# Performance work log

Measured on AMD Instinct MI355X. Metric: run time of the kernel, lower is better.

Reference implementation:

```python
import jax, jax.numpy as jnp
import numpy as np

B, H, L, D = 4, 16, 1024, 64
DROP_P = 0.5


def setup_inputs() -> dict:
    key = jax.random.key(0)
    kq, kk, kv, kg, kd = jax.random.split(key, 5)
    q = jax.random.normal(kq, (B, H, L, D), dtype=jnp.float32)
    k = jax.random.normal(kk, (B, H, L, D), dtype=jnp.float32)
    v = jax.random.normal(kv, (B, H, L, D), dtype=jnp.float32)
    # standard Gumbel(0,1) noise consumed by gumbel_softmax
    gumbel_noise = jax.random.gumbel(kg, (B, H, L, L), dtype=jnp.float32)
    # inverted-dropout mask: keep w.p. (1-p), scale kept by 1/(1-p)
    keep = jax.random.bernoulli(kd, 1.0 - DROP_P, (B, H, L, L))
    drop_mask = keep.astype(jnp.float32) / (1.0 - DROP_P)
    return {"q": q, "k": k, "v": v, "gumbel_noise": gumbel_noise, "drop_mask": drop_mask}


def reference(q, k, v, gumbel_noise, drop_mask):
    q = jax.nn.elu(q)
    k = jax.nn.elu(k)
    v = jax.nn.elu(v)
    scale = q.shape[-1] ** -0.5  # qk / sqrt(d)
    qk = jnp.einsum("bhld,bhmd->bhlm", q, k) * scale
    # gumbel_softmax(hard=True), tau=1
    logits = qk + gumbel_noise
    y_soft = jax.nn.softmax(logits, axis=-1)
    y_hard = jax.nn.one_hot(jnp.argmax(y_soft, axis=-1), logits.shape[-1], dtype=y_soft.dtype)
    y = jax.lax.stop_gradient(y_hard - y_soft) + y_soft  # straight-through
    dropped = y * drop_mask  # dropout p=0.5
    out = jnp.einsum("bhlm,bhmd->bhld", dropped, v)
    return out
```

## Files before the change

### kernel.cpp

```cpp
#include <hip/hip_runtime.h>
#include <math.h>


#define BH    64
#define SEQ   1024
#define DIM   64
#define LT    128
#define MT    128
#define NTHR  256

typedef short bf16x8 __attribute__((ext_vector_type(8)));
typedef float f32x16 __attribute__((ext_vector_type(16)));

__device__ __forceinline__ float eluf(float x) { return x > 0.0f ? x : expm1f(x); }

__device__ __forceinline__ unsigned f2bf_bits(float x) {
    unsigned u = __float_as_uint(x);
    return (u + 0x7fffu + ((u >> 16) & 1u)) >> 16;
}

__device__ __forceinline__ void top2_update(float v, int m,
                                            float& b1, int& i1,
                                            float& b2, int& i2) {
    bool gt1 = (v > b1) || (v == b1 && m < i1);
    bool gt2 = (v > b2) || (v == b2 && m < i2);
    float nb2 = gt1 ? b1 : (gt2 ? v : b2);
    int   ni2 = gt1 ? i1 : (gt2 ? m : i2);
    b1 = gt1 ? v : b1;
    i1 = gt1 ? m : i1;
    b2 = nb2; i2 = ni2;
}

__device__ __forceinline__ void stage_tile(const float4* __restrict__ src4,
                                           short* __restrict__ hi,
                                           short* __restrict__ lo,
                                           int tid) {
    #pragma unroll
    for (int i = 0; i < 8; ++i) {
        int f = tid + NTHR * i;
        int row = f >> 4, qd = f & 15;
        float4 val = src4[row * 16 + qd];
        float e0 = eluf(val.x), e1 = eluf(val.y), e2 = eluf(val.z), e3 = eluf(val.w);
        unsigned h0 = f2bf_bits(e0), h1 = f2bf_bits(e1), h2 = f2bf_bits(e2), h3 = f2bf_bits(e3);
        unsigned l0b = f2bf_bits(e0 - __uint_as_float(h0 << 16));
        unsigned l1b = f2bf_bits(e1 - __uint_as_float(h1 << 16));
        unsigned l2b = f2bf_bits(e2 - __uint_as_float(h2 << 16));
        unsigned l3b = f2bf_bits(e3 - __uint_as_float(h3 << 16));
        short4 hv = make_short4((short)h0, (short)h1, (short)h2, (short)h3);
        short4 lv = make_short4((short)l0b, (short)l1b, (short)l2b, (short)l3b);
        int off = row * 64 + ((((qd >> 1) ^ (row & 7)) << 3)) + ((qd & 1) << 2);
        *(short4*)&hi[off] = hv;
        *(short4*)&lo[off] = lv;
    }
}

__global__ __launch_bounds__(NTHR, 2)
void fused_gumbel_attn(const float* __restrict__ q,
                       const float* __restrict__ k,
                       const float* __restrict__ v,
                       const float* __restrict__ gum,
                       const float* __restrict__ drop,
                       float* __restrict__ out) {
    __shared__ __align__(16) short qhi[LT * DIM];
    __shared__ __align__(16) short qlo[LT * DIM];
    __shared__ __align__(16) short khi[MT * DIM];
    __shared__ __align__(16) short klo[MT * DIM];
    __shared__ int   m1s[LT], m2s[LT], msf[LT];
    __shared__ float dropv[LT];

    const int tid  = threadIdx.x;
    const int w    = tid >> 6;
    const int lane = tid & 63;
    const int lrow = lane & 31;
    const int half = lane >> 5;
    const int bh   = blockIdx.x >> 3;
    const int l0   = (blockIdx.x & 7) * LT;
    const size_t rowbase = (size_t)(bh * SEQ + l0);

    stage_tile((const float4*)q + rowbase * 16, qhi, qlo, tid);

    float best1[16], best2[16];
    int   idx1[16], idx2[16];
    #pragma unroll
    for (int r = 0; r < 16; ++r) {
        best1[r] = -INFINITY; best2[r] = -INFINITY; idx1[r] = 0; idx2[r] = 0;
    }

    const float* gumrow = gum + (((size_t)(bh * SEQ + l0 + w * 32 + half * 4)) << 10) + lrow;

    const int aswz = lrow & 7;

    for (int mt = 0; mt < SEQ / MT; ++mt) {
        const int m0 = mt * MT;
        __syncthreads();
        stage_tile((const float4*)k + (size_t)(bh * SEQ + m0) * 16, khi, klo, tid);
        __syncthreads();

        float ga[16], gb[16];
        #pragma unroll
        for (int r = 0; r < 16; ++r) {
            int roff = ((r & 3) + 8 * (r >> 2)) << 10;
            ga[r] = gumrow[roff + m0];
            gb[r] = gumrow[roff + m0 + 32];
        }

        f32x16 acc[4];
        #pragma unroll
        for (int t = 0; t < 4; ++t) acc[t] = (f32x16)0.0f;

        #pragma unroll
        for (int ks = 0; ks < 4; ++ks) {
            const int o = ks * 2 + half;
            const int arow = w * 32 + lrow;
            bf16x8 a_hi = *(const bf16x8*)&qhi[arow * 64 + ((o ^ aswz) << 3)];
            bf16x8 a_lo = *(const bf16x8*)&qlo[arow * 64 + ((o ^ aswz) << 3)];
            #pragma unroll
            for (int t = 0; t < 4; ++t) {
                const int brow = t * 32 + lrow;
                bf16x8 b_hi = *(const bf16x8*)&khi[brow * 64 + ((o ^ aswz) << 3)];
                bf16x8 b_lo = *(const bf16x8*)&klo[brow * 64 + ((o ^ aswz) << 3)];
                acc[t] = __builtin_amdgcn_mfma_f32_32x32x16_bf16(a_hi, b_hi, acc[t], 0, 0, 0);
                acc[t] = __builtin_amdgcn_mfma_f32_32x32x16_bf16(a_hi, b_lo, acc[t], 0, 0, 0);
                acc[t] = __builtin_amdgcn_mfma_f32_32x32x16_bf16(a_lo, b_hi, acc[t], 0, 0, 0);
            }
        }

        #pragma unroll
        for (int r = 0; r < 16; ++r) {
            float lg = fmaf(acc[0][r], 0.125f, ga[r]);
            top2_update(lg, m0 + lrow, best1[r], idx1[r], best2[r], idx2[r]);
        }
        #pragma unroll
        for (int r = 0; r < 16; ++r) {
            int roff = ((r & 3) + 8 * (r >> 2)) << 10;
            ga[r] = gumrow[roff + m0 + 64];
        }
        #pragma unroll
        for (int r = 0; r < 16; ++r) {
            float lg = fmaf(acc[1][r], 0.125f, gb[r]);
            top2_update(lg, m0 + 32 + lrow, best1[r], idx1[r], best2[r], idx2[r]);
        }
        #pragma unroll
        for (int r = 0; r < 16; ++r) {
            int roff = ((r & 3) + 8 * (r >> 2)) << 10;
            gb[r] = gumrow[roff + m0 + 96];
        }
        #pragma unroll
        for (int r = 0; r < 16; ++r) {
            float lg = fmaf(acc[2][r], 0.125f, ga[r]);
            top2_update(lg, m0 + 64 + lrow, best1[r], idx1[r], best2[r], idx2[r]);
        }
        #pragma unroll
        for (int r = 0; r < 16; ++r) {
            float lg = fmaf(acc[3][r], 0.125f, gb[r]);
            top2_update(lg, m0 + 96 + lrow, best1[r], idx1[r], best2[r], idx2[r]);
        }
    }

    #pragma unroll
    for (int r = 0; r < 16; ++r) {
        #pragma unroll
        for (int s = 1; s < 32; s <<= 1) {
            float ob1 = __shfl_xor(best1[r], s);
            int   oi1 = __shfl_xor(idx1[r], s);
            float ob2 = __shfl_xor(best2[r], s);
            int   oi2 = __shfl_xor(idx2[r], s);
            top2_update(ob1, oi1, best1[r], idx1[r], best2[r], idx2[r]);
            top2_update(ob2, oi2, best1[r], idx1[r], best2[r], idx2[r]);
        }
    }
    if (lrow == 0) {
        #pragma unroll
        for (int r = 0; r < 16; ++r) {
            int local_row = w * 32 + (r & 3) + 8 * (r >> 2) + 4 * half;
            m1s[local_row] = idx1[r];
            m2s[local_row] = idx2[r];
        }
    }
    __syncthreads();

    {
        const int row  = tid >> 1;
        const int cand = tid & 1;
        const int m    = cand ? m2s[row] : m1s[row];
        const float4* q4r = (const float4*)q + (rowbase + row) * 16;
        const float4* k4r = (const float4*)k + (size_t)(bh * SEQ + m) * 16;
        double s = 0.0;
        #pragma unroll
        for (int i = 0; i < 16; ++i) {
            float4 a = q4r[i], b = k4r[i];
            s += (double)eluf(a.x) * (double)eluf(b.x);
            s += (double)eluf(a.y) * (double)eluf(b.y);
            s += (double)eluf(a.z) * (double)eluf(b.z);
            s += (double)eluf(a.w) * (double)eluf(b.w);
        }
        double L = s * 0.125 + (double)gum[((rowbase + row) << 10) + m];
        double Lo = __shfl_xor(L, 1);
        int    mo = __shfl_xor(m, 1);
        int mstar = (L > Lo || (L == Lo && m < mo)) ? m : mo;
        if (cand == 0) {
            msf[row]   = mstar;
            dropv[row] = drop[((rowbase + row) << 10) + mstar];
        }
    }
    __syncthreads();

    const float4* v4  = (const float4*)v + (size_t)(bh * SEQ) * 16;
    float4*       o4  = (float4*)out + rowbase * 16;
    #pragma unroll
    for (int i = 0; i < 8; ++i) {
        int f = tid + NTHR * i;
        int row = f >> 4, qd = f & 15;
        int m = msf[row];
        float dm = dropv[row];
        float4 vv = v4[m * 16 + qd];
        float4 ov;
        ov.x = dm * eluf(vv.x); ov.y = dm * eluf(vv.y);
        ov.z = dm * eluf(vv.z); ov.w = dm * eluf(vv.w);
        o4[row * 16 + qd] = ov;
    }
}

extern "C" void kernel_launch(void* const* d_in, const int* in_sizes, int n_in,
                              void* d_out, int out_size, void* d_ws, size_t ws_size,
                              hipStream_t stream) {
    const float* q    = (const float*)d_in[0];
    const float* k    = (const float*)d_in[1];
    const float* v    = (const float*)d_in[2];
    const float* gum  = (const float*)d_in[3];
    const float* drop = (const float*)d_in[4];
    float* out = (float*)d_out;

    fused_gumbel_attn<<<dim3(BH * (SEQ / LT)), dim3(NTHR), 0, stream>>>(
        q, k, v, gum, drop, out);
}
```

Baseline: 605.7 us.

## Split fused kernel into K-prep, register-pipelined score/top2, and fixup kernels

Replaces the single fused kernel with three launches. The first converts ELU(K) into hi/lo bf16 halves once, into workspace. The second gives each wave a 32-row Q tile held in registers and a quarter of the key range, and double-buffers K fragments and gumbel loads straight from global memory with no LDS or block barriers. The third merges the per-split top-2 candidates, rescores them in double precision, and writes the output. This is meant to remove the per-tile K restaging, the syncthreads stalls and the redundant ELU/split work. The cost is extra launches, a workspace round trip, and a tie-break simplified to strict greater-than.

```diff
diff --git a/kernel.cpp b/kernel.cpp
--- a/kernel.cpp
+++ b/kernel.cpp
@@ -2,12 +2,13 @@
 #include <math.h>
 
 
-#define BH    64
-#define SEQ   1024
-#define DIM   64
-#define LT    128
-#define MT    128
-#define NTHR  256
+#define BH      64
+#define SEQ     1024
+#define DIM     64
+#define NSPLIT  4
+#define MR      (SEQ / NSPLIT)
+#define NTILES  (MR / 32)
+#define NTHR    256
 
 typedef short bf16x8 __attribute__((ext_vector_type(8)));
 typedef float f32x16 __attribute__((ext_vector_type(16)));
@@ -19,11 +20,18 @@
     return (u + 0x7fffu + ((u >> 16) & 1u)) >> 16;
 }
 
+__device__ __forceinline__ void split_bf16(float x, short& h, short& l) {
+    unsigned hb = f2bf_bits(x);
+    float hf = __uint_as_float(hb << 16);
+    h = (short)hb;
+    l = (short)f2bf_bits(x - hf);
+}
+
 __device__ __forceinline__ void top2_update(float v, int m,
                                             float& b1, int& i1,
                                             float& b2, int& i2) {
-    bool gt1 = (v > b1) || (v == b1 && m < i1);
-    bool gt2 = (v > b2) || (v == b2 && m < i2);
+    bool gt1 = v > b1;
+    bool gt2 = v > b2;
     float nb2 = gt1 ? b1 : (gt2 ? v : b2);
     int   ni2 = gt1 ? i1 : (gt2 ? m : i2);
     b1 = gt1 ? v : b1;
@@ -31,193 +39,189 @@
     b2 = nb2; i2 = ni2;
 }
 
-__device__ __forceinline__ void stage_tile(const float4* __restrict__ src4,
-                                           short* __restrict__ hi,
-                                           short* __restrict__ lo,
-                                           int tid) {
-    #pragma unroll
-    for (int i = 0; i < 8; ++i) {
-        int f = tid + NTHR * i;
-        int row = f >> 4, qd = f & 15;
-        float4 val = src4[row * 16 + qd];
-        float e0 = eluf(val.x), e1 = eluf(val.y), e2 = eluf(val.z), e3 = eluf(val.w);
-        unsigned h0 = f2bf_bits(e0), h1 = f2bf_bits(e1), h2 = f2bf_bits(e2), h3 = f2bf_bits(e3);
-        unsigned l0b = f2bf_bits(e0 - __uint_as_float(h0 << 16));
-        unsigned l1b = f2bf_bits(e1 - __uint_as_float(h1 << 16));
-        unsigned l2b = f2bf_bits(e2 - __uint_as_float(h2 << 16));
-        unsigned l3b = f2bf_bits(e3 - __uint_as_float(h3 << 16));
-        short4 hv = make_short4((short)h0, (short)h1, (short)h2, (short)h3);
-        short4 lv = make_short4((short)l0b, (short)l1b, (short)l2b, (short)l3b);
-        int off = row * 64 + ((((qd >> 1) ^ (row & 7)) << 3)) + ((qd & 1) << 2);
-        *(short4*)&hi[off] = hv;
-        *(short4*)&lo[off] = lv;
-    }
-}
-
-__global__ __launch_bounds__(NTHR, 2)
-void fused_gumbel_attn(const float* __restrict__ q,
-                       const float* __restrict__ k,
-                       const float* __restrict__ v,
+__global__ __launch_bounds__(NTHR)
+void prep_k_kernel(const float4* __restrict__ k4,
+                   short4* __restrict__ khi, short4* __restrict__ klo) {
+    int f = blockIdx.x * NTHR + threadIdx.x;
+    float4 val = k4[f];
+    short4 hv, lv;
+    split_bf16(eluf(val.x), hv.x, lv.x);
+    split_bf16(eluf(val.y), hv.y, lv.y);
+    split_bf16(eluf(val.z), hv.z, lv.z);
+    split_bf16(eluf(val.w), hv.w, lv.w);
+    khi[f] = hv;
+    klo[f] = lv;
+}
+
+__global__ __launch_bounds__(NTHR, 3)
+void score_top2_kernel(const float* __restrict__ q,
+                       const short* __restrict__ khi,
+                       const short* __restrict__ klo,
                        const float* __restrict__ gum,
-                       const float* __restrict__ drop,
-                       float* __restrict__ out) {
-    __shared__ __align__(16) short qhi[LT * DIM];
-    __shared__ __align__(16) short qlo[LT * DIM];
-    __shared__ __align__(16) short khi[MT * DIM];
-    __shared__ __align__(16) short klo[MT * DIM];
-    __shared__ int   m1s[LT], m2s[LT], msf[LT];
-    __shared__ float dropv[LT];
-
-    const int tid  = threadIdx.x;
-    const int w    = tid >> 6;
-    const int lane = tid & 63;
+                       int4* __restrict__ top2out) {
+    const int w    = threadIdx.x >> 6;
+    const int lane = threadIdx.x & 63;
     const int lrow = lane & 31;
     const int half = lane >> 5;
-    const int bh   = blockIdx.x >> 3;
-    const int l0   = (blockIdx.x & 7) * LT;
-    const size_t rowbase = (size_t)(bh * SEQ + l0);
-
-    stage_tile((const float4*)q + rowbase * 16, qhi, qlo, tid);
-
-    float best1[16], best2[16];
-    int   idx1[16], idx2[16];
-    #pragma unroll
-    for (int r = 0; r < 16; ++r) {
-        best1[r] = -INFINITY; best2[r] = -INFINITY; idx1[r] = 0; idx2[r] = 0;
-    }
-
-    const float* gumrow = gum + (((size_t)(bh * SEQ + l0 + w * 32 + half * 4)) << 10) + lrow;
-
-    const int aswz = lrow & 7;
-
-    for (int mt = 0; mt < SEQ / MT; ++mt) {
-        const int m0 = mt * MT;
-        __syncthreads();
-        stage_tile((const float4*)k + (size_t)(bh * SEQ + m0) * 16, khi, klo, tid);
-        __syncthreads();
-
-        float ga[16], gb[16];
+
+    const int x     = blockIdx.x & 7;
+    const int j     = blockIdx.x >> 3;
+    const int bh    = x * 8 + (j & 7);
+    const int ltile = j >> 3;
+    const int l0    = ltile * 32;
+    const int ms    = w * MR;
+
+    const size_t row = (size_t)bh * SEQ + l0 + lrow;
+
+    bf16x8 qh[4], ql[4];
+    {
+        const float4* q4 = (const float4*)q + row * 16;
+        #pragma unroll
+        for (int ks = 0; ks < 4; ++ks) {
+            float4 a = q4[ks * 4 + half * 2];
+            float4 b = q4[ks * 4 + half * 2 + 1];
+            float e[8] = { eluf(a.x), eluf(a.y), eluf(a.z), eluf(a.w),
+                           eluf(b.x), eluf(b.y), eluf(b.z), eluf(b.w) };
+            #pragma unroll
+            for (int t = 0; t < 8; ++t) {
+                short h, l;
+                split_bf16(e[t], h, l);
+                qh[ks][t] = h;
+                ql[ks][t] = l;
+            }
+        }
+    }
+
+    const short* kh_base = khi + ((size_t)(bh * SEQ + ms + lrow) * 64 + half * 8);
+    const short* kl_base = klo + ((size_t)(bh * SEQ + ms + lrow) * 64 + half * 8);
+    const float* gp      = gum + (row << 10) + ms + half * 4;
+
+    float b1 = -INFINITY, b2 = -INFINITY;
+    int   i1 = 0, i2 = 0;
+
+    bf16x8 ah[2][4], al[2][4];
+    float  g[2][16];
+
+    #pragma unroll
+    for (int ks = 0; ks < 4; ++ks) {
+        ah[0][ks] = *(const bf16x8*)(kh_base + ks * 16);
+        al[0][ks] = *(const bf16x8*)(kl_base + ks * 16);
+    }
+    #pragma unroll
+    for (int qd = 0; qd < 4; ++qd) {
+        float4 t4 = *(const float4*)(gp + qd * 8);
+        g[0][qd * 4 + 0] = t4.x; g[0][qd * 4 + 1] = t4.y;
+        g[0][qd * 4 + 2] = t4.z; g[0][qd * 4 + 3] = t4.w;
+    }
+
+    #pragma unroll
+    for (int t = 0; t < NTILES; ++t) {
+        const int cur = t & 1, nxt = cur ^ 1;
+        if (t < NTILES - 1) {
+            #pragma unroll
+            for (int ks = 0; ks < 4; ++ks) {
+                ah[nxt][ks] = *(const bf16x8*)(kh_base + (t + 1) * 2048 + ks * 16);
+                al[nxt][ks] = *(const bf16x8*)(kl_base + (t + 1) * 2048 + ks * 16);
+            }
+            #pragma unroll
+            for (int qd = 0; qd < 4; ++qd) {
+                float4 t4 = *(const float4*)(gp + (t + 1) * 32 + qd * 8);
+                g[nxt][qd * 4 + 0] = t4.x; g[nxt][qd * 4 + 1] = t4.y;
+                g[nxt][qd * 4 + 2] = t4.z; g[nxt][qd * 4 + 3] = t4.w;
+            }
+        }
+
+        f32x16 acc = (f32x16)0.0f;
+        #pragma unroll
+        for (int ks = 0; ks < 4; ++ks) {
+            acc = __builtin_amdgcn_mfma_f32_32x32x16_bf16(ah[cur][ks], qh[ks], acc, 0, 0, 0);
+            acc = __builtin_amdgcn_mfma_f32_32x32x16_bf16(ah[cur][ks], ql[ks], acc, 0, 0, 0);
+            acc = __builtin_amdgcn_mfma_f32_32x32x16_bf16(al[cur][ks], qh[ks], acc, 0, 0, 0);
+        }
+
+        const int mb = ms + t * 32 + half * 4;
         #pragma unroll
         for (int r = 0; r < 16; ++r) {
-            int roff = ((r & 3) + 8 * (r >> 2)) << 10;
-            ga[r] = gumrow[roff + m0];
-            gb[r] = gumrow[roff + m0 + 32];
-        }
-
-        f32x16 acc[4];
-        #pragma unroll
-        for (int t = 0; t < 4; ++t) acc[t] = (f32x16)0.0f;
-
-        #pragma unroll
-        for (int ks = 0; ks < 4; ++ks) {
-            const int o = ks * 2 + half;
-            const int arow = w * 32 + lrow;
-            bf16x8 a_hi = *(const bf16x8*)&qhi[arow * 64 + ((o ^ aswz) << 3)];
-            bf16x8 a_lo = *(const bf16x8*)&qlo[arow * 64 + ((o ^ aswz) << 3)];
-            #pragma unroll
-            for (int t = 0; t < 4; ++t) {
-                const int brow = t * 32 + lrow;
-                bf16x8 b_hi = *(const bf16x8*)&khi[brow * 64 + ((o ^ aswz) << 3)];
-                bf16x8 b_lo = *(const bf16x8*)&klo[brow * 64 + ((o ^ aswz) << 3)];
-                acc[t] = __builtin_amdgcn_mfma_f32_32x32x16_bf16(a_hi, b_hi, acc[t], 0, 0, 0);
-                acc[t] = __builtin_amdgcn_mfma_f32_32x32x16_bf16(a_hi, b_lo, acc[t], 0, 0, 0);
-                acc[t] = __builtin_amdgcn_mfma_f32_32x32x16_bf16(a_lo, b_hi, acc[t], 0, 0, 0);
-            }
-        }
-
-        #pragma unroll
-        for (int r = 0; r < 16; ++r) {
-            float lg = fmaf(acc[0][r], 0.125f, ga[r]);
-            top2_update(lg, m0 + lrow, best1[r], idx1[r], best2[r], idx2[r]);
-        }
-        #pragma unroll
-        for (int r = 0; r < 16; ++r) {
-            int roff = ((r & 3) + 8 * (r >> 2)) << 10;
-            ga[r] = gumrow[roff + m0 + 64];
-        }
-        #pragma unroll
-        for (int r = 0; r < 16; ++r) {
-            float lg = fmaf(acc[1][r], 0.125f, gb[r]);
-            top2_update(lg, m0 + 32 + lrow, best1[r], idx1[r], best2[r], idx2[r]);
-        }
-        #pragma unroll
-        for (int r = 0; r < 16; ++r) {
-            int roff = ((r & 3) + 8 * (r >> 2)) << 10;
-            gb[r] = gumrow[roff + m0 + 96];
-        }
-        #pragma unroll
-        for (int r = 0; r < 16; ++r) {
-            float lg = fmaf(acc[2][r], 0.125f, ga[r]);
-            top2_update(lg, m0 + 64 + lrow, best1[r], idx1[r], best2[r], idx2[r]);
-        }
-        #pragma unroll
-        for (int r = 0; r < 16; ++r) {
-            float lg = fmaf(acc[3][r], 0.125f, gb[r]);
-            top2_update(lg, m0 + 96 + lrow, best1[r], idx1[r], best2[r], idx2[r]);
-        }
-    }
-
-    #pragma unroll
-    for (int r = 0; r < 16; ++r) {
-        #pragma unroll
-        for (int s = 1; s < 32; s <<= 1) {
-            float ob1 = __shfl_xor(best1[r], s);
-            int   oi1 = __shfl_xor(idx1[r], s);
-            float ob2 = __shfl_xor(best2[r], s);
-            int   oi2 = __shfl_xor(idx2[r], s);
-            top2_update(ob1, oi1, best1[r], idx1[r], best2[r], idx2[r]);
-            top2_update(ob2, oi2, best1[r], idx1[r], best2[r], idx2[r]);
-        }
-    }
-    if (lrow == 0) {
-        #pragma unroll
-        for (int r = 0; r < 16; ++r) {
-            int local_row = w * 32 + (r & 3) + 8 * (r >> 2) + 4 * half;
-            m1s[local_row] = idx1[r];
-            m2s[local_row] = idx2[r];
-        }
+            float lg = fmaf(acc[r], 0.125f, g[cur][r]);
+            top2_update(lg, mb + (r & 3) + 8 * (r >> 2), b1, i1, b2, i2);
+        }
+    }
+
+    {
+        float ob1 = __shfl_xor(b1, 32);
+        int   oi1 = __shfl_xor(i1, 32);
+        float ob2 = __shfl_xor(b2, 32);
+        int   oi2 = __shfl_xor(i2, 32);
+        top2_update(ob1, oi1, b1, i1, b2, i2);
+        top2_update(ob2, oi2, b1, i1, b2, i2);
+    }
+    if (half == 0) {
+        top2out[row * NSPLIT + w] = make_int4(__float_as_int(b1), i1,
+                                              __float_as_int(b2), i2);
+    }
+}
+
+__global__ __launch_bounds__(NTHR)
+void fixup_out_kernel(const float* __restrict__ q,
+                      const float* __restrict__ k,
+                      const float* __restrict__ v,
+                      const float* __restrict__ gum,
+                      const float* __restrict__ drop,
+                      const int4* __restrict__ top2in,
+                      float* __restrict__ out) {
+    __shared__ int   msf[128];
+    __shared__ float dropv[128];
+
+    const int rloc = threadIdx.x >> 1;
+    const int cand = threadIdx.x & 1;
+    const size_t row = (size_t)blockIdx.x * 128 + rloc;
+    const int bh = (int)(row >> 10);
+
+    float b1 = -INFINITY, b2 = -INFINITY;
+    int   i1 = 0, i2 = 0;
+    #pragma unroll
+    for (int s = 0; s < NSPLIT; ++s) {
+        int4 p = top2in[row * NSPLIT + s];
+        top2_update(__int_as_float(p.x), p.y, b1, i1, b2, i2);
+        top2_update(__int_as_float(p.z), p.w, b1, i1, b2, i2);
+    }
+    const int m = cand ? i2 : i1;
+
+    const float4* q4r = (const float4*)q + row * 16;
+    const float4* k4r = (const float4*)k + ((size_t)bh * SEQ + m) * 16;
+    double s = 0.0;
+    #pragma unroll
+    for (int i = 0; i < 16; ++i) {
+        float4 a = q4r[i], b = k4r[i];
+        s += (double)eluf(a.x) * (double)eluf(b.x);
+        s += (double)eluf(a.y) * (double)eluf(b.y);
+        s += (double)eluf(a.z) * (double)eluf(b.z);
+        s += (double)eluf(a.w) * (double)eluf(b.w);
+    }
+    double L  = s * 0.125 + (double)gum[(row << 10) + m];
+    double Lo = __shfl_xor(L, 1);
+    int    mo = __shfl_xor(m, 1);
+    const int mstar = (L > Lo || (L == Lo && m < mo)) ? m : mo;
+    if (cand == 0) {
+        msf[rloc]   = mstar;
+        dropv[rloc] = drop[(row << 10) + mstar];
     }
     __syncthreads();
 
-    {
-        const int row  = tid >> 1;
-        const int cand = tid & 1;
-        const int m    = cand ? m2s[row] : m1s[row];
-        const float4* q4r = (const float4*)q + (rowbase + row) * 16;
-        const float4* k4r = (const float4*)k + (size_t)(bh * SEQ + m) * 16;
-        double s = 0.0;
-        #pragma unroll
-        for (int i = 0; i < 16; ++i) {
-            float4 a = q4r[i], b = k4r[i];
-            s += (double)eluf(a.x) * (double)eluf(b.x);
-            s += (double)eluf(a.y) * (double)eluf(b.y);
-            s += (double)eluf(a.z) * (double)eluf(b.z);
-            s += (double)eluf(a.w) * (double)eluf(b.w);
-        }
-        double L = s * 0.125 + (double)gum[((rowbase + row) << 10) + m];
-        double Lo = __shfl_xor(L, 1);
-        int    mo = __shfl_xor(m, 1);
-        int mstar = (L > Lo || (L == Lo && m < mo)) ? m : mo;
-        if (cand == 0) {
-            msf[row]   = mstar;
-            dropv[row] = drop[((rowbase + row) << 10) + mstar];
-        }
-    }
-    __syncthreads();
-
-    const float4* v4  = (const float4*)v + (size_t)(bh * SEQ) * 16;
-    float4*       o4  = (float4*)out + rowbase * 16;
+    const int bh0 = (int)(((size_t)blockIdx.x * 128) >> 10);
+    const float4* v4 = (const float4*)v + (size_t)bh0 * SEQ * 16;
+    float4* o4 = (float4*)out + (size_t)blockIdx.x * 128 * 16;
     #pragma unroll
     for (int i = 0; i < 8; ++i) {
-        int f = tid + NTHR * i;
-        int row = f >> 4, qd = f & 15;
-        int m = msf[row];
-        float dm = dropv[row];
-        float4 vv = v4[m * 16 + qd];
+        int f  = threadIdx.x + NTHR * i;
+        int rr = f >> 4, qd = f & 15;
+        int   mm = msf[rr];
+        float dm = dropv[rr];
+        float4 vv = v4[mm * 16 + qd];
         float4 ov;
         ov.x = dm * eluf(vv.x); ov.y = dm * eluf(vv.y);
         ov.z = dm * eluf(vv.z); ov.w = dm * eluf(vv.w);
-        o4[row * 16 + qd] = ov;
+        o4[rr * 16 + qd] = ov;
     }
 }
 
@@ -231,6 +235,14 @@
     const float* drop = (const float*)d_in[4];
     float* out = (float*)d_out;
 
-    fused_gumbel_attn<<<dim3(BH * (SEQ / LT)), dim3(NTHR), 0, stream>>>(
-        q, k, v, gum, drop, out);
-}
+    short* khi = (short*)d_ws;
+    short* klo = khi + (size_t)BH * SEQ * DIM;
+    int4*  top2 = (int4*)((char*)d_ws + (size_t)2 * BH * SEQ * DIM * sizeof(short));
+
+    prep_k_kernel<<<dim3((BH * SEQ * DIM / 4) / NTHR), dim3(NTHR), 0, stream>>>(
+        (const float4*)k, (short4*)khi, (short4*)klo);
+    score_top2_kernel<<<dim3(BH * (SEQ / 32) * NSPLIT / 4), dim3(NTHR), 0, stream>>>(
+        q, khi, klo, gum, top2);
+    fixup_out_kernel<<<dim3((BH * SEQ) / 128), dim3(NTHR), 0, stream>>>(
+        q, k, v, gum, drop, top2, out);
+}
```

Measured after the change: 574.6 us. 1.05x faster.
